# Kernel tuning notes

Measured on AMD Instinct MI355X. Metric: run time of the kernel, lower is better.

Reference implementation:

```python
import jax, jax.numpy as jnp
import numpy as np

B, S, E, H, HD, M = 4, 2048, 2048, 16, 128, 8192
EPS = 1e-5
SQRT_2_OVER_PI = 0.7978845608028654


def layer_norm(x, g, b):
    mu = jnp.mean(x, axis=-1, keepdims=True)
    var = jnp.mean(jnp.square(x - mu), axis=-1, keepdims=True)
    return (x - mu) * jax.lax.rsqrt(var + EPS) * g + b


def gelu_new(x):
    # tanh-approximate GELU (HF 'gelu_new')
    return 0.5 * x * (1.0 + jnp.tanh(SQRT_2_OVER_PI * (x + 0.044715 * x * x * x)))


def setup_inputs() -> dict:
    key = jax.random.key(0)
    ks = jax.random.split(key, 6)
    std = 0.02
    x = jax.random.normal(ks[0], (B, S, E), dtype=jnp.float32)
    mask = jnp.tril(jnp.ones((S, S), dtype=jnp.float32))  # causal, 1=allowed
    Wqkv = jax.random.normal(ks[1], (E, 3, H, HD), dtype=jnp.float32) * std
    bqkv = jnp.zeros((3, H, HD), dtype=jnp.float32)
    Wo = jax.random.normal(ks[2], (H, HD, E), dtype=jnp.float32) * std
    bo = jnp.zeros((E,), dtype=jnp.float32)
    Wfc = jax.random.normal(ks[3], (E, M), dtype=jnp.float32) * std
    bfc = jnp.zeros((M,), dtype=jnp.float32)
    Wp = jax.random.normal(ks[4], (M, E), dtype=jnp.float32) * std
    bp = jnp.zeros((E,), dtype=jnp.float32)
    return {
        'x': x, 'mask': mask,
        'ln1_g': jnp.ones((E,), jnp.float32), 'ln1_b': jnp.zeros((E,), jnp.float32),
        'Wqkv': Wqkv, 'bqkv': bqkv, 'Wo': Wo, 'bo': bo,
        'ln2_g': jnp.ones((E,), jnp.float32), 'ln2_b': jnp.zeros((E,), jnp.float32),
        'Wfc': Wfc, 'bfc': bfc, 'Wp': Wp, 'bp': bp,
        'layer_idx': 0,
    }


def reference(x, mask, ln1_g, ln1_b, Wqkv, bqkv, Wo, bo, ln2_g, ln2_b, Wfc, bfc, Wp, bp, layer_idx):
    # --- attention branch ---
    h = layer_norm(x, ln1_g, ln1_b)
    qkv = jnp.einsum('bse,ethd->btshd', h, Wqkv) + bqkv[:, None, :, :]  # [3,B?] -> actually [b,t,s,h,d]
    q, k, v = qkv[:, 0], qkv[:, 1], qkv[:, 2]  # each [b,s,h,d]
    scale = jax.lax.rsqrt(float(HD))  # scale_by_inverse_layer_idx=False
    q = q * scale
    scores = jnp.einsum('bqhd,bkhd->bhqk', q, k)
    scores = scores + (1.0 - mask) * -1e9  # mask broadcasts [q,k]
    w = jax.nn.softmax(scores, axis=-1).astype(x.dtype)  # dropout: inference, p=0
    attn = jnp.einsum('bhqk,bkhd->bqhd', w, v)
    attn = jnp.einsum('bqhd,hde->bqe', attn, Wo) + bo
    x = x + attn
    # --- MLP branch ---
    h2 = layer_norm(x, ln2_g, ln2_b)
    ff = gelu_new(jnp.einsum('bse,em->bsm', h2, Wfc) + bfc)
    ff = jnp.einsum('bsm,me->bse', ff, Wp) + bp
    return x + ff
```

## Files before the change

### kernel.cpp

```cpp
#include <hip/hip_runtime.h>
#include <hip/hip_bf16.h>
#include <math.h>


typedef __bf16 bf16;
typedef __attribute__((ext_vector_type(8))) __bf16 bf16x8;
typedef __attribute__((ext_vector_type(4))) float f32x4;

#define GLOBAL_AS __attribute__((address_space(1)))
#define LDS_AS __attribute__((address_space(3)))

__device__ __forceinline__ void gl_lds16(const bf16* g, bf16* l) {
  __builtin_amdgcn_global_load_lds((const GLOBAL_AS void*)g, (LDS_AS void*)l, 16, 0, 0);
}

struct Acc { f32x4 v[4][4]; };

__device__ __forceinline__ void gemm_core(const bf16* __restrict__ A, long lda,
                                          const bf16* __restrict__ Bt, long ldb,
                                          int m0, int n0, int kbeg, int kend,
                                          bf16* sa, bf16* sb, Acc& acc) {
  const int t    = threadIdx.x;
  const int lane = t & 63;
  const int w    = t >> 6;
  const int wm   = (w >> 1) << 6;
  const int wn   = (w & 1) << 6;
  const int quad = lane >> 4;
  const int l15  = lane & 15;
  const int rowA = t >> 2;
  const int kc   = (t & 3) << 3;

#pragma unroll
  for (int i = 0; i < 4; i++)
#pragma unroll
    for (int j = 0; j < 4; j++)
      acc.v[i][j] = f32x4{0.f, 0.f, 0.f, 0.f};

  bf16* sa_w0 = &sa[(w << 6) * 8];
  bf16* sa_w1 = &sa[(256 + (w << 6)) * 8];
  bf16* sb_w0 = &sb[(w << 6) * 8];
  bf16* sb_w1 = &sb[(256 + (w << 6)) * 8];

  for (int k0 = kbeg; k0 < kend; k0 += 32) {
    const bf16* ga = A + (long)(m0 + rowA) * lda + (k0 + kc);
    const bf16* gb = Bt + (long)(n0 + rowA) * ldb + (k0 + kc);
    gl_lds16(ga, sa_w0);
    gl_lds16(ga + 64 * lda, sa_w1);
    gl_lds16(gb, sb_w0);
    gl_lds16(gb + 64 * ldb, sb_w1);
    __syncthreads();

    bf16x8 af[4], bfv[4];
#pragma unroll
    for (int i = 0; i < 4; i++)
      af[i] = *(const bf16x8*)&sa[(wm + i * 16 + l15) * 32 + quad * 8];
#pragma unroll
    for (int j = 0; j < 4; j++)
      bfv[j] = *(const bf16x8*)&sb[(wn + j * 16 + l15) * 32 + quad * 8];
#pragma unroll
    for (int i = 0; i < 4; i++)
#pragma unroll
      for (int j = 0; j < 4; j++)
        acc.v[i][j] = __builtin_amdgcn_mfma_f32_16x16x32_bf16(af[i], bfv[j], acc.v[i][j], 0, 0, 0);
    __syncthreads();
  }
}

template <typename F>
__device__ __forceinline__ void epilogue(int m0, int n0, const Acc& acc, F f) {
  const int t = threadIdx.x;
  const int lane = t & 63;
  const int w = t >> 6;
  const int wm = (w >> 1) << 6, wn = (w & 1) << 6;
  const int quad = lane >> 4, l15 = lane & 15;
#pragma unroll
  for (int i = 0; i < 4; i++)
#pragma unroll
    for (int j = 0; j < 4; j++)
#pragma unroll
      for (int r = 0; r < 4; r++)
        f(m0 + wm + i * 16 + quad * 4 + r, n0 + wn + j * 16 + l15, acc.v[i][j][r]);
}

__global__ void k_transpose_cast(const float* __restrict__ src, bf16* __restrict__ dst,
                                 int R, int C) {
  __shared__ float tile[32][33];
  const int c0 = blockIdx.x << 5, r0 = blockIdx.y << 5;
  const int tx = threadIdx.x, ty = threadIdx.y;
  for (int i = ty; i < 32; i += 8)
    tile[i][tx] = src[(long)(r0 + i) * C + (c0 + tx)];
  __syncthreads();
  for (int i = ty; i < 32; i += 8)
    dst[(long)(c0 + i) * R + (r0 + tx)] = (bf16)tile[tx][i];
}

__global__ void k_layernorm(const float* __restrict__ x, const float* __restrict__ g,
                            const float* __restrict__ bta, bf16* __restrict__ out) {
  __shared__ float red[8];
  const long row = blockIdx.x;
  const float* xr = x + row * 2048;
  const int t = threadIdx.x;
  float4 a = reinterpret_cast<const float4*>(xr)[t];
  float4 b4 = reinterpret_cast<const float4*>(xr)[t + 256];
  float va[8] = {a.x, a.y, a.z, a.w, b4.x, b4.y, b4.z, b4.w};
  float s = 0.f, ss = 0.f;
#pragma unroll
  for (int i = 0; i < 8; i++) { s += va[i]; ss += va[i] * va[i]; }
#pragma unroll
  for (int o = 32; o > 0; o >>= 1) { s += __shfl_xor(s, o, 64); ss += __shfl_xor(ss, o, 64); }
  if ((t & 63) == 0) { red[t >> 6] = s; red[4 + (t >> 6)] = ss; }
  __syncthreads();
  s = red[0] + red[1] + red[2] + red[3];
  ss = red[4] + red[5] + red[6] + red[7];
  const float mu = s * (1.f / 2048.f);
  const float rstd = rsqrtf(ss * (1.f / 2048.f) - mu * mu + 1e-5f);
  bf16* op = out + row * 2048;
#pragma unroll
  for (int c = 0; c < 4; c++) {
    int i0 = t * 4 + c;
    op[i0] = (bf16)((va[c] - mu) * rstd * g[i0] + bta[i0]);
    int i1 = 1024 + t * 4 + c;
    op[i1] = (bf16)((va[4 + c] - mu) * rstd * g[i1] + bta[i1]);
  }
}

__global__ __launch_bounds__(256, 2) void k_gemm_qkv(
    const bf16* __restrict__ A, const bf16* __restrict__ Bt, const float* __restrict__ bias,
    bf16* __restrict__ q, bf16* __restrict__ k, bf16* __restrict__ v) {
  __shared__ bf16 sa[128 * 32], sb[128 * 32];
  const int m0 = blockIdx.y << 7, n0 = blockIdx.x << 7;
  Acc acc;
  gemm_core(A, 2048, Bt, 2048, m0, n0, 0, 2048, sa, sb, acc);
  epilogue(m0, n0, acc, [&](int row, int col, float val) {
    float vv = val + bias[col];
    const int which = col >> 11, hh = (col >> 7) & 15, d = col & 127;
    if (which == 0)
      q[((long)hh * 2048 + row) * 128 + d] = (bf16)(vv * 0.08838834764831845f);
    else if (which == 1)
      k[((long)hh * 2048 + row) * 128 + d] = (bf16)vv;
    else
      v[((long)hh * 128 + d) * 2048 + row] = (bf16)vv;
  });
}

#define SC_HEAD 2228224L

__global__ __launch_bounds__(256, 2) void k_gemm_scores(
    const bf16* __restrict__ q, const bf16* __restrict__ kk, bf16* __restrict__ sc) {
  const int idx = blockIdx.x;
  int m = (int)((sqrtf(8.f * idx + 1.f) - 1.f) * 0.5f);
  if ((m + 1) * (m + 2) / 2 <= idx) m++;
  if (m * (m + 1) / 2 > idx) m--;
  const int n = idx - m * (m + 1) / 2;
  const int h = blockIdx.z;
  __shared__ bf16 sa[128 * 32], sb[128 * 32];
  const bf16* qb = q + (long)h * 2048 * 128;
  const bf16* kb = kk + (long)h * 2048 * 128;
  Acc acc;
  gemm_core(qb, 128, kb, 128, m << 7, n << 7, 0, 128, sa, sb, acc);
  const long lda_m = (long)(m + 1) << 7;
  bf16* scp = sc + (long)h * SC_HEAD + (long)m * (m + 1) * 8192;
  const int mbase = m << 7;
  epilogue(m << 7, n << 7, acc, [&](int row, int col, float val) {
    scp[(long)(row - mbase) * lda_m + col] = (bf16)val;
  });
}

__global__ void k_softmax(bf16* __restrict__ sc) {
  __shared__ float red[8];
  const int sq = blockIdx.x, h = blockIdx.y;
  const int mb = sq >> 7;
  const int lda = (mb + 1) << 7;
  bf16* rowp = sc + (long)h * SC_HEAD + (long)mb * (mb + 1) * 8192 + (long)(sq & 127) * lda;
  const int L = sq + 1;
  const int Lpad = lda;
  const int t = threadIdx.x;
  float v[8];
  float mx = -3e38f;
#pragma unroll
  for (int i = 0; i < 8; i++) {
    int idx = t + (i << 8);
    v[i] = (idx < L) ? (float)rowp[idx] : -3e38f;
    mx = fmaxf(mx, v[i]);
  }
#pragma unroll
  for (int o = 32; o > 0; o >>= 1) mx = fmaxf(mx, __shfl_xor(mx, o, 64));
  if ((t & 63) == 0) red[t >> 6] = mx;
  __syncthreads();
  mx = fmaxf(fmaxf(red[0], red[1]), fmaxf(red[2], red[3]));
  float sum = 0.f;
#pragma unroll
  for (int i = 0; i < 8; i++) {
    int idx = t + (i << 8);
    if (idx < L) { v[i] = __expf(v[i] - mx); sum += v[i]; }
  }
#pragma unroll
  for (int o = 32; o > 0; o >>= 1) sum += __shfl_xor(sum, o, 64);
  if ((t & 63) == 0) red[4 + (t >> 6)] = sum;
  __syncthreads();
  sum = red[4] + red[5] + red[6] + red[7];
  const float inv = 1.f / sum;
#pragma unroll
  for (int i = 0; i < 8; i++) {
    int idx = t + (i << 8);
    if (idx < L) rowp[idx] = (bf16)(v[i] * inv);
    else if (idx < Lpad) rowp[idx] = (bf16)0.f;
  }
}

__global__ __launch_bounds__(256, 2) void k_gemm_pv(
    const bf16* __restrict__ sc, const bf16* __restrict__ v, bf16* __restrict__ attn) {
  __shared__ bf16 sa[128 * 32], sb[128 * 32];
  const int mb = blockIdx.x;
  const int h = blockIdx.y;
  const int lda = (mb + 1) << 7;
  const bf16* A = sc + (long)h * SC_HEAD + (long)mb * (mb + 1) * 8192;
  const bf16* Bt = v + (long)h * 128 * 2048;
  Acc acc;
  gemm_core(A, lda, Bt, 2048, 0, 0, 0, lda, sa, sb, acc);
  const int rbase = mb << 7;
  epilogue(0, 0, acc, [&](int row, int col, float val) {
    attn[((long)(rbase + row) * 16 + h) * 128 + col] = (bf16)val;
  });
}

__global__ __launch_bounds__(256, 2) void k_gemm_wo(
    const bf16* __restrict__ A, const bf16* __restrict__ Bt, const float* __restrict__ bias,
    const float* __restrict__ xin, float* __restrict__ x1) {
  __shared__ bf16 sa[128 * 32], sb[128 * 32];
  const int m0 = blockIdx.y << 7, n0 = blockIdx.x << 7;
  Acc acc;
  gemm_core(A, 2048, Bt, 2048, m0, n0, 0, 2048, sa, sb, acc);
  epilogue(m0, n0, acc, [&](int row, int col, float val) {
    long idx = (long)row * 2048 + col;
    x1[idx] = xin[idx] + val + bias[col];
  });
}

__global__ __launch_bounds__(256, 2) void k_gemm_fc(
    const bf16* __restrict__ A, const bf16* __restrict__ Bt, const float* __restrict__ bias,
    bf16* __restrict__ ff) {
  __shared__ bf16 sa[128 * 32], sb[128 * 32];
  const int m0 = blockIdx.y << 7, n0 = blockIdx.x << 7;
  Acc acc;
  gemm_core(A, 2048, Bt, 2048, m0, n0, 0, 2048, sa, sb, acc);
  epilogue(m0, n0, acc, [&](int row, int col, float val) {
    float u = val + bias[col];
    float cc = 0.7978845608028654f * (u + 0.044715f * u * u * u);
    float ge = 0.5f * u * (1.f + tanhf(cc));
    ff[(long)row * 8192 + col] = (bf16)ge;
  });
}

__global__ __launch_bounds__(256, 2) void k_gemm_wp(
    const bf16* __restrict__ A, const bf16* __restrict__ Bt, const float* __restrict__ bias,
    float* __restrict__ out) {
  __shared__ bf16 sa[128 * 32], sb[128 * 32];
  const int m0 = blockIdx.y << 7, n0 = blockIdx.x << 7;
  Acc acc;
  gemm_core(A, 8192, Bt, 8192, m0, n0, 0, 8192, sa, sb, acc);
  epilogue(m0, n0, acc, [&](int row, int col, float val) {
    long idx = (long)row * 2048 + col;
    out[idx] = out[idx] + val + bias[col];
  });
}

extern "C" void kernel_launch(void* const* d_in, const int* in_sizes, int n_in,
                              void* d_out, int out_size, void* d_ws, size_t ws_size,
                              hipStream_t stream) {
  const float* x     = (const float*)d_in[0];
  const float* ln1_g = (const float*)d_in[2];
  const float* ln1_b = (const float*)d_in[3];
  const float* Wqkv  = (const float*)d_in[4];
  const float* bqkv  = (const float*)d_in[5];
  const float* Wo    = (const float*)d_in[6];
  const float* bo    = (const float*)d_in[7];
  const float* ln2_g = (const float*)d_in[8];
  const float* ln2_b = (const float*)d_in[9];
  const float* Wfc   = (const float*)d_in[10];
  const float* bfc   = (const float*)d_in[11];
  const float* Wp    = (const float*)d_in[12];
  const float* bp    = (const float*)d_in[13];
  float* out = (float*)d_out;

  char* p = (char*)d_ws;
  bf16* WqkvT = (bf16*)p; p += 6144L * 2048 * 2;
  bf16* WoT   = (bf16*)p; p += 2048L * 2048 * 2;
  bf16* WfcT  = (bf16*)p; p += 8192L * 2048 * 2;
  bf16* WpT   = (bf16*)p; p += 2048L * 8192 * 2;
  bf16* h     = (bf16*)p; p += 8192L * 2048 * 2;
  bf16* qb    = (bf16*)p; p += 16L * 2048 * 128 * 2;
  bf16* kb    = (bf16*)p; p += 16L * 2048 * 128 * 2;
  bf16* vb    = (bf16*)p; p += 16L * 2048 * 128 * 2;
  bf16* attnb = (bf16*)p; p += 16L * 2048 * 128 * 2;
  bf16* sc    = (bf16*)p; p += 16L * SC_HEAD * 2;
  bf16* h2 = h;
  bf16* ff = sc;

  dim3 tb(32, 8);
  k_transpose_cast<<<dim3(192, 64), tb, 0, stream>>>(Wqkv, WqkvT, 2048, 6144);
  k_transpose_cast<<<dim3(64, 64), tb, 0, stream>>>(Wo, WoT, 2048, 2048);
  k_transpose_cast<<<dim3(256, 64), tb, 0, stream>>>(Wfc, WfcT, 2048, 8192);
  k_transpose_cast<<<dim3(64, 256), tb, 0, stream>>>(Wp, WpT, 8192, 2048);

  k_layernorm<<<8192, 256, 0, stream>>>(x, ln1_g, ln1_b, h);

  for (int b = 0; b < 4; b++) {
    const bf16* hb = h + (long)b * 2048 * 2048;
    k_gemm_qkv<<<dim3(48, 16), 256, 0, stream>>>(hb, WqkvT, bqkv, qb, kb, vb);
    k_gemm_scores<<<dim3(136, 1, 16), 256, 0, stream>>>(qb, kb, sc);
    k_softmax<<<dim3(2048, 16), 256, 0, stream>>>(sc);
    k_gemm_pv<<<dim3(16, 16), 256, 0, stream>>>(sc, vb, attnb);
    k_gemm_wo<<<dim3(16, 16), 256, 0, stream>>>(attnb, WoT, bo,
                                                x + (long)b * 2048 * 2048,
                                                out + (long)b * 2048 * 2048);
  }

  k_layernorm<<<8192, 256, 0, stream>>>(out, ln2_g, ln2_b, h2);

  for (int r = 0; r < 2; r++) {
    const bf16* h2r = h2 + (long)r * 4096 * 2048;
    k_gemm_fc<<<dim3(64, 32), 256, 0, stream>>>(h2r, WfcT, bfc, ff);
    k_gemm_wp<<<dim3(16, 32), 256, 0, stream>>>(ff, WpT, bp, out + (long)r * 4096 * 2048);
  }
}
```

Before: 2.018 ms.

## Use 256x256 double-buffered swizzled GEMM for QKV, FC and projection

Adds a new GEMM core with 256x256 tiles, 512 threads, BK=64 double-buffered async global-to-LDS loads, an XOR-swizzled LDS layout and raised wave priority around MFMA. It also adds a block-index swizzle for L2 locality. QKV, FC and the output projection now use this core. The MLP runs as single FC and projection launches over all 8192 rows, with the ff buffer remapped onto the region freed by the attention buffers. The aim is higher arithmetic intensity and less LDS and sync overhead. The cost is 128 KB of LDS per block, which may limit occupancy, and some tile-quantization waste on the QKV grid.

New measurement: 1.931 ms. 1.04x faster.

```diff
diff --git a/kernel.cpp b/kernel.cpp
--- a/kernel.cpp
+++ b/kernel.cpp
@@ -12,6 +12,110 @@
 
 __device__ __forceinline__ void gl_lds16(const bf16* g, bf16* l) {
   __builtin_amdgcn_global_load_lds((const GLOBAL_AS void*)g, (LDS_AS void*)l, 16, 0, 0);
+}
+
+#define MFMA16 __builtin_amdgcn_mfma_f32_16x16x32_bf16
+
+__device__ __forceinline__ void gemm256_core(const bf16* __restrict__ A, long lda,
+                                             const bf16* __restrict__ Bt, long ldb,
+                                             int m0, int n0, int K,
+                                             f32x4 (&acc)[8][4]) {
+  __shared__ bf16 lds[65536];
+  const int t = threadIdx.x;
+  const int lane = t & 63;
+  const int w = t >> 6;
+  const int wm = (w >> 2) << 7;
+  const int wn = (w & 3) << 6;
+  const int quad = lane >> 4;
+  const int l15 = lane & 15;
+
+#pragma unroll
+  for (int i = 0; i < 8; i++)
+#pragma unroll
+    for (int j = 0; j < 4; j++) acc[i][j] = f32x4{0.f, 0.f, 0.f, 0.f};
+
+  const int axor = (l15 & 7) << 3;
+  const int c0 = (quad << 3) ^ axor;
+  const int aroff = (wm + l15) << 6;
+  const int broff = (wn + l15) << 6;
+
+  const int srow = (w << 3) + (lane >> 3);
+  const int scol = ((lane & 7) ^ (lane >> 3)) << 3;
+  const bf16* gA = A + (long)(m0 + srow) * lda + scol;
+  const bf16* gB = Bt + (long)(n0 + srow) * ldb + scol;
+  const int sdst = w << 9;
+
+  const int NK = K >> 6;
+
+  auto stage = [&](int buf, int kt) {
+    const bf16* ga = gA + (long)kt * 64;
+    const bf16* gb = gB + (long)kt * 64;
+    bf16* da = lds + buf * 16384 + sdst;
+    bf16* db = lds + 32768 + buf * 16384 + sdst;
+#pragma unroll
+    for (int c = 0; c < 4; c++) gl_lds16(ga + (long)(c * 64) * lda, da + c * 4096);
+#pragma unroll
+    for (int c = 0; c < 4; c++) gl_lds16(gb + (long)(c * 64) * ldb, db + c * 4096);
+  };
+
+  stage(0, 0);
+  if (NK > 1) stage(1, 1);
+
+  for (int kt = 0; kt < NK; ++kt) {
+    const int cur = kt & 1;
+    const bf16* sa = lds + cur * 16384;
+    const bf16* sb = lds + 32768 + cur * 16384;
+
+    if (kt + 1 < NK) asm volatile("s_waitcnt vmcnt(8)" ::: "memory");
+    else             asm volatile("s_waitcnt vmcnt(0)" ::: "memory");
+    __builtin_amdgcn_sched_barrier(0);
+    __builtin_amdgcn_s_barrier();
+    asm volatile("" ::: "memory");
+
+    bf16x8 b0[4], b1[4];
+#pragma unroll
+    for (int j = 0; j < 4; j++) {
+      b0[j] = *(const bf16x8*)&sb[broff + j * 1024 + c0];
+      b1[j] = *(const bf16x8*)&sb[broff + j * 1024 + (c0 ^ 32)];
+    }
+#pragma unroll
+    for (int p = 0; p < 4; p++) {
+      bf16x8 a00 = *(const bf16x8*)&sa[aroff + (2 * p + 0) * 1024 + c0];
+      bf16x8 a01 = *(const bf16x8*)&sa[aroff + (2 * p + 0) * 1024 + (c0 ^ 32)];
+      bf16x8 a10 = *(const bf16x8*)&sa[aroff + (2 * p + 1) * 1024 + c0];
+      bf16x8 a11 = *(const bf16x8*)&sa[aroff + (2 * p + 1) * 1024 + (c0 ^ 32)];
+      __builtin_amdgcn_s_setprio(1);
+#pragma unroll
+      for (int j = 0; j < 4; j++) {
+        acc[2 * p + 0][j] = MFMA16(a00, b0[j], acc[2 * p + 0][j], 0, 0, 0);
+        acc[2 * p + 0][j] = MFMA16(a01, b1[j], acc[2 * p + 0][j], 0, 0, 0);
+        acc[2 * p + 1][j] = MFMA16(a10, b0[j], acc[2 * p + 1][j], 0, 0, 0);
+        acc[2 * p + 1][j] = MFMA16(a11, b1[j], acc[2 * p + 1][j], 0, 0, 0);
+      }
+      __builtin_amdgcn_s_setprio(0);
+    }
+
+    asm volatile("" ::: "memory");
+    __builtin_amdgcn_s_barrier();
+    asm volatile("" ::: "memory");
+    if (kt + 2 < NK) stage(cur, kt + 2);
+  }
+}
+
+template <typename F>
+__device__ __forceinline__ void epilogue256(int m0, int n0, const f32x4 (&acc)[8][4], F f) {
+  const int t = threadIdx.x;
+  const int lane = t & 63;
+  const int w = t >> 6;
+  const int wm = (w >> 2) << 7, wn = (w & 3) << 6;
+  const int quad = lane >> 4, l15 = lane & 15;
+#pragma unroll
+  for (int i = 0; i < 8; i++)
+#pragma unroll
+    for (int j = 0; j < 4; j++)
+#pragma unroll
+      for (int r = 0; r < 4; r++)
+        f(m0 + wm + i * 16 + quad * 4 + r, n0 + wn + j * 16 + l15, acc[i][j][r]);
 }
 
 struct Acc { f32x4 v[4][4]; };
@@ -61,7 +165,7 @@
     for (int i = 0; i < 4; i++)
 #pragma unroll
       for (int j = 0; j < 4; j++)
-        acc.v[i][j] = __builtin_amdgcn_mfma_f32_16x16x32_bf16(af[i], bfv[j], acc.v[i][j], 0, 0, 0);
+        acc.v[i][j] = MFMA16(af[i], bfv[j], acc.v[i][j], 0, 0, 0);
     __syncthreads();
   }
 }
@@ -124,14 +228,15 @@
   }
 }
 
-__global__ __launch_bounds__(256, 2) void k_gemm_qkv(
+__global__ __launch_bounds__(512, 2) void k_qkv256(
     const bf16* __restrict__ A, const bf16* __restrict__ Bt, const float* __restrict__ bias,
     bf16* __restrict__ q, bf16* __restrict__ k, bf16* __restrict__ v) {
-  __shared__ bf16 sa[128 * 32], sb[128 * 32];
-  const int m0 = blockIdx.y << 7, n0 = blockIdx.x << 7;
-  Acc acc;
-  gemm_core(A, 2048, Bt, 2048, m0, n0, 0, 2048, sa, sb, acc);
-  epilogue(m0, n0, acc, [&](int row, int col, float val) {
+  const int bid = blockIdx.x;
+  const int swz = (bid & 7) * 24 + (bid >> 3);
+  const int tx = swz % 24, ty = swz / 24;
+  f32x4 acc[8][4];
+  gemm256_core(A, 2048, Bt, 2048, ty << 8, tx << 8, 2048, acc);
+  epilogue256(ty << 8, tx << 8, acc, [&](int row, int col, float val) {
     float vv = val + bias[col];
     const int which = col >> 11, hh = (col >> 7) & 15, d = col & 127;
     if (which == 0)
@@ -237,29 +342,30 @@
   });
 }
 
-__global__ __launch_bounds__(256, 2) void k_gemm_fc(
+__global__ __launch_bounds__(512, 2) void k_fc256(
     const bf16* __restrict__ A, const bf16* __restrict__ Bt, const float* __restrict__ bias,
     bf16* __restrict__ ff) {
-  __shared__ bf16 sa[128 * 32], sb[128 * 32];
-  const int m0 = blockIdx.y << 7, n0 = blockIdx.x << 7;
-  Acc acc;
-  gemm_core(A, 2048, Bt, 2048, m0, n0, 0, 2048, sa, sb, acc);
-  epilogue(m0, n0, acc, [&](int row, int col, float val) {
+  const int bid = blockIdx.x;
+  const int swz = (bid & 7) * 128 + (bid >> 3);
+  const int tx = swz & 31, ty = swz >> 5;
+  f32x4 acc[8][4];
+  gemm256_core(A, 2048, Bt, 2048, ty << 8, tx << 8, 2048, acc);
+  epilogue256(ty << 8, tx << 8, acc, [&](int row, int col, float val) {
     float u = val + bias[col];
     float cc = 0.7978845608028654f * (u + 0.044715f * u * u * u);
-    float ge = 0.5f * u * (1.f + tanhf(cc));
-    ff[(long)row * 8192 + col] = (bf16)ge;
-  });
-}
-
-__global__ __launch_bounds__(256, 2) void k_gemm_wp(
+    ff[(long)row * 8192 + col] = (bf16)(0.5f * u * (1.f + tanhf(cc)));
+  });
+}
+
+__global__ __launch_bounds__(512, 2) void k_wp256(
     const bf16* __restrict__ A, const bf16* __restrict__ Bt, const float* __restrict__ bias,
     float* __restrict__ out) {
-  __shared__ bf16 sa[128 * 32], sb[128 * 32];
-  const int m0 = blockIdx.y << 7, n0 = blockIdx.x << 7;
-  Acc acc;
-  gemm_core(A, 8192, Bt, 8192, m0, n0, 0, 8192, sa, sb, acc);
-  epilogue(m0, n0, acc, [&](int row, int col, float val) {
+  const int bid = blockIdx.x;
+  const int swz = (bid & 7) * 32 + (bid >> 3);
+  const int tx = swz & 7, ty = swz >> 3;
+  f32x4 acc[8][4];
+  gemm256_core(A, 8192, Bt, 8192, ty << 8, tx << 8, 8192, acc);
+  epilogue256(ty << 8, tx << 8, acc, [&](int row, int col, float val) {
     long idx = (long)row * 2048 + col;
     out[idx] = out[idx] + val + bias[col];
   });
@@ -284,18 +390,19 @@
   float* out = (float*)d_out;
 
   char* p = (char*)d_ws;
-  bf16* WqkvT = (bf16*)p; p += 6144L * 2048 * 2;
-  bf16* WoT   = (bf16*)p; p += 2048L * 2048 * 2;
   bf16* WfcT  = (bf16*)p; p += 8192L * 2048 * 2;
   bf16* WpT   = (bf16*)p; p += 2048L * 8192 * 2;
   bf16* h     = (bf16*)p; p += 8192L * 2048 * 2;
+  char* ffreg = p;
+  bf16* WqkvT = (bf16*)p; p += 6144L * 2048 * 2;
+  bf16* WoT   = (bf16*)p; p += 2048L * 2048 * 2;
   bf16* qb    = (bf16*)p; p += 16L * 2048 * 128 * 2;
   bf16* kb    = (bf16*)p; p += 16L * 2048 * 128 * 2;
   bf16* vb    = (bf16*)p; p += 16L * 2048 * 128 * 2;
   bf16* attnb = (bf16*)p; p += 16L * 2048 * 128 * 2;
   bf16* sc    = (bf16*)p; p += 16L * SC_HEAD * 2;
   bf16* h2 = h;
-  bf16* ff = sc;
+  bf16* ff = (bf16*)ffreg;
 
   dim3 tb(32, 8);
   k_transpose_cast<<<dim3(192, 64), tb, 0, stream>>>(Wqkv, WqkvT, 2048, 6144);
@@ -307,7 +414,7 @@
 
   for (int b = 0; b < 4; b++) {
     const bf16* hb = h + (long)b * 2048 * 2048;
-    k_gemm_qkv<<<dim3(48, 16), 256, 0, stream>>>(hb, WqkvT, bqkv, qb, kb, vb);
+    k_qkv256<<<dim3(192), 512, 0, stream>>>(hb, WqkvT, bqkv, qb, kb, vb);
     k_gemm_scores<<<dim3(136, 1, 16), 256, 0, stream>>>(qb, kb, sc);
     k_softmax<<<dim3(2048, 16), 256, 0, stream>>>(sc);
     k_gemm_pv<<<dim3(16, 16), 256, 0, stream>>>(sc, vb, attnb);
@@ -318,9 +425,6 @@
 
   k_layernorm<<<8192, 256, 0, stream>>>(out, ln2_g, ln2_b, h2);
 
-  for (int r = 0; r < 2; r++) {
-    const bf16* h2r = h2 + (long)r * 4096 * 2048;
-    k_gemm_fc<<<dim3(64, 32), 256, 0, stream>>>(h2r, WfcT, bfc, ff);
-    k_gemm_wp<<<dim3(16, 32), 256, 0, stream>>>(ff, WpT, bp, out + (long)r * 4096 * 2048);
-  }
-}
+  k_fc256<<<dim3(1024), 512, 0, stream>>>(h2, WfcT, bfc, ff);
+  k_wp256<<<dim3(256), 512, 0, stream>>>(ff, WpT, bp, out);
+}
```
